# Optimization experiments

Measured on AMD Instinct MI355X. Metric: run time of the kernel, lower is better.

## Reference

```python
import jax, jax.numpy as jnp
import numpy as np

C_IN, C_OUT, K = 64, 64, 3
KK = K * K


def _conv3x3(x, w, b):
    # x: [B, Cin, H, W], w: [Cout, Cin, 3, 3], b: [Cout] or None. stride 1, pad 1.
    y = jax.lax.conv_general_dilated(
        x, w, window_strides=(1, 1), padding=((1, 1), (1, 1)),
        dimension_numbers=("NCHW", "OIHW", "NCHW"))
    if b is not None:
        y = y + b[None, :, None, None]
    return y


def _deform_conv2d(x, offset, mask, weight):
    # torchvision.ops.deform_conv2d with stride=1, pad=1, dilation=1, 1 offset group.
    # x: [B,C,H,W]; offset: [B,2*KK,H,W] (per-tap (dy,dx)); mask: [B,KK,H,W];
    # weight: [O,C,K,K]
    B, C, H, W = x.shape
    O = weight.shape[0]
    ky, kx = jnp.meshgrid(jnp.arange(K), jnp.arange(K), indexing="ij")
    hs = jnp.arange(H)
    ws = jnp.arange(W)
    # base sample positions per tap k=(ky*K+kx): [KK,H,W]
    base_y = (hs[:, None] - 1)[None] + ky.reshape(KK, 1, 1)
    base_x = (ws[None, :] - 1)[None] + kx.reshape(KK, 1, 1)
    off = offset.reshape(B, KK, 2, H, W)
    py = base_y[None].astype(x.dtype) + off[:, :, 0]  # [B,KK,H,W]
    px = base_x[None].astype(x.dtype) + off[:, :, 1]

    y0 = jnp.floor(py)
    x0 = jnp.floor(px)
    wy = py - y0  # bilinear fractional weights
    wx = px - x0
    y0i = y0.astype(jnp.int32)
    x0i = x0.astype(jnp.int32)

    imflat = x.reshape(B, C, H * W)

    def gather_b(im, idx):  # im: [C,HW], idx: [KK,H,W] -> [C,KK,H,W]
        return im[:, idx]

    val = jnp.zeros((B, C, KK, H, W), x.dtype)
    for dy, dx in ((0, 0), (0, 1), (1, 0), (1, 1)):
        yc = y0i + dy
        xc = x0i + dx
        valid = ((yc >= 0) & (yc < H) & (xc >= 0) & (xc < W)).astype(x.dtype)
        cw = (wy if dy else (1.0 - wy)) * (wx if dx else (1.0 - wx)) * valid
        idx = jnp.clip(yc, 0, H - 1) * W + jnp.clip(xc, 0, W - 1)
        g = jax.vmap(gather_b)(imflat, idx)  # [B,C,KK,H,W]
        val = val + cw[:, None] * g
    val = val * mask[:, None]  # modulation
    # contract 9-tap patches with conv weight
    return jnp.einsum("bckhw,ock->bohw", val, weight.reshape(O, C, KK))


def setup_inputs() -> dict:
    key = jax.random.key(0)
    ks = jax.random.split(key, 8)
    B, H, W = 4, 96, 96
    cin2 = 2 * C_IN + 2
    frame_i = jax.random.normal(ks[0], (B, C_IN, H, W), jnp.float32)
    frame_j = jax.random.normal(ks[1], (B, C_IN, H, W), jnp.float32)
    flow_ij = jax.random.normal(ks[2], (B, 2, H, W), jnp.float32)
    # small random weights so offsets are nonzero (zero-init would degenerate)
    w_off = jax.random.normal(ks[3], (2 * KK, cin2, K, K), jnp.float32) * 0.01
    b_off = jax.random.normal(ks[4], (2 * KK,), jnp.float32) * 0.1
    w_mod = jax.random.normal(ks[5], (KK, cin2, K, K), jnp.float32) * 0.01
    b_mod = jax.random.normal(ks[6], (KK,), jnp.float32) * 0.1
    w_reg = jax.random.normal(ks[7], (C_OUT, C_IN, K, K), jnp.float32) * (1.0 / np.sqrt(C_IN * KK))
    return {"frame_i": frame_i, "frame_j": frame_j, "flow_ij": flow_ij,
            "w_off": w_off, "b_off": b_off, "w_mod": w_mod, "b_mod": b_mod,
            "w_reg": w_reg}


def reference(frame_i, frame_j, flow_ij, w_off, b_off, w_mod, b_mod, w_reg):
    offset_input = jnp.concatenate([frame_i, frame_j, flow_ij], axis=1)
    offset = _conv3x3(offset_input, w_off, b_off)            # [B,2*KK,H,W]
    modulator = 2.0 * jax.nn.sigmoid(_conv3x3(offset_input, w_mod, b_mod))  # [B,KK,H,W]
    return _deform_conv2d(frame_j, offset, modulator, w_reg)
```

## Files before the change

### kernel.cpp

```cpp
#include <hip/hip_runtime.h>
#include <math.h>

#define BB   4
#define HH   96
#define WW   96
#define HW   (HH * WW)
#define CIN  64
#define COUT 64
#define C2B  192
#define NROW (BB * HW)
#define ZROW NROW
#define NSTRIP (NROW / 16)
#define BPX3 (NSTRIP / 8)
#define NA   (9 * 5 * 2 * 512)
#define NW   (9 * 2 * 4 * 512)
#define PXB2 (NROW / 32)
#define PWBLK 324
#define TSX  35
#define RS   20

typedef short v8s __attribute__((ext_vector_type(8)));
typedef float v4f __attribute__((ext_vector_type(4)));

__device__ __forceinline__ unsigned short f2bf(float f) {
    unsigned u = __float_as_uint(f);
    return (unsigned short)((u + 0x7FFFu + ((u >> 16) & 1u)) >> 16);
}
__device__ __forceinline__ unsigned pack2(float a, float b) {
    return (unsigned)f2bf(a) | ((unsigned)f2bf(b) << 16);
}
__device__ __forceinline__ unsigned bil2(unsigned a, unsigned b, unsigned c,
                                         unsigned d, float w00, float w01,
                                         float w10, float w11) {
    float lo = w00 * __uint_as_float(a << 16) + w01 * __uint_as_float(b << 16)
             + w10 * __uint_as_float(c << 16) + w11 * __uint_as_float(d << 16);
    float hi = w00 * __uint_as_float(a & 0xffff0000u)
             + w01 * __uint_as_float(b & 0xffff0000u)
             + w10 * __uint_as_float(c & 0xffff0000u)
             + w11 * __uint_as_float(d & 0xffff0000u);
    return pack2(lo, hi);
}

__global__ __launch_bounds__(256) void prep_kernel(
    const float* __restrict__ fi, const float* __restrict__ fj,
    const float* __restrict__ fl, const float* __restrict__ w_off,
    const float* __restrict__ w_mod, const float* __restrict__ w_reg,
    unsigned short* __restrict__ xt, unsigned short* __restrict__ wa2f,
    unsigned short* __restrict__ wb2f)
{
    int blk = blockIdx.x;
    if (blk < PXB2) {
        __shared__ __align__(16) unsigned tile[64 * TSX];
        int tid = threadIdx.x;
        int p = tid & 63, cg = tid >> 6;
        int u = blk >> 1, half = blk & 1;
        int r0 = u * 64;
        int b = r0 / HW;
        int hw = r0 - b * HW + p;
        uint4* dst = (uint4*)(xt + (size_t)r0 * C2B);
        if (half == 0) {
            const float* pi = fi + (size_t)b * CIN * HW + hw;
#pragma unroll
            for (int d = 0; d < 8; ++d) {
                int c = cg * 16 + 2 * d;
                tile[p * TSX + cg * 8 + d] =
                    pack2(pi[(size_t)c * HW], pi[(size_t)(c + 1) * HW]);
            }
            __syncthreads();
#pragma unroll
            for (int i = 0; i < 2; ++i) {
                int gq = i * 256 + tid;
                int rl = gq >> 3, c4 = gq & 7;
                const unsigned* s = &tile[rl * TSX + c4 * 4];
                uint4 v = {s[0], s[1], s[2], s[3]};
                dst[rl * 24 + c4] = v;
            }
        } else {
            const float* pj = fj + (size_t)b * CIN * HW + hw;
#pragma unroll
            for (int d = 0; d < 8; ++d) {
                int c = cg * 16 + 2 * d;
                tile[p * TSX + cg * 8 + d] =
                    pack2(pj[(size_t)c * HW], pj[(size_t)(c + 1) * HW]);
            }
            if (cg == 0) {
                const float* pf = fl + (size_t)b * 2 * HW + hw;
                tile[p * TSX + 32] = pack2(pf[0], pf[HW]);
            }
            __syncthreads();
#pragma unroll
            for (int i = 0; i < 4; ++i) {
                int gq = i * 256 + tid;
                int rl = gq >> 4, c4 = gq & 15;
                uint4 v = {0u, 0u, 0u, 0u};
                if (c4 < 8) {
                    const unsigned* s = &tile[rl * TSX + c4 * 4];
                    v.x = s[0]; v.y = s[1]; v.z = s[2]; v.w = s[3];
                } else if (c4 == 8) {
                    v.x = tile[rl * TSX + 32];
                }
                dst[rl * 24 + 8 + c4] = v;
            }
        }
    } else if (blk < PXB2 + PWBLK) {
        int e = (blk - PXB2) * 256 + threadIdx.x;
        if (e < NA) {
            int t  = e / 5120;
            int r1 = e - t * 5120;
            int ks = r1 >> 10;
            int r2 = r1 & 1023;
            int nt = r2 >> 9;
            int l9 = r2 & 511;
            int l  = l9 >> 3, ee = l9 & 7;
            int m  = l & 15, g = l >> 4;
            int oc = nt * 16 + m;
            int ch = ks * 32 + g * 8 + ee;
            float v = 0.0f;
            if (oc < 27 && ch < 130) {
                if (oc < 18) v = w_off[((size_t)oc * 130 + ch) * 9 + t];
                else         v = w_mod[((size_t)(oc - 18) * 130 + ch) * 9 + t];
            }
            wa2f[e] = f2bf(v);
        } else {
            int e2 = e - NA;
            if (e2 < NW) {
                int k  = e2 >> 12;
                int r1 = e2 & 4095;
                int ks = r1 >> 11;
                int r2 = r1 & 2047;
                int nt = r2 >> 9;
                int l9 = r2 & 511;
                int l  = l9 >> 3, ee = l9 & 7;
                int m  = l & 15, g = l >> 4;
                int o  = nt * 16 + m;
                int c  = ks * 32 + g * 8 + ee;
                wb2f[e2] = f2bf(w_reg[((size_t)o * 64 + c) * 9 + k]);
            }
        }
    } else {
        if (threadIdx.x < 24) {
            uint4 z = {0u, 0u, 0u, 0u};
            ((uint4*)(xt + (size_t)ZROW * C2B))[threadIdx.x] = z;
        }
    }
}

__global__ __launch_bounds__(256, 2) void fused_kernel(
    const unsigned short* __restrict__ xt,
    const unsigned short* __restrict__ wa2f,
    const unsigned short* __restrict__ wb2f,
    const float* __restrict__ b_off, const float* __restrict__ b_mod,
    float* __restrict__ out)
{
    __shared__ float lraw[16 * 28];
    __shared__ __align__(16) float red[4][64 * RS];

    int l = threadIdx.x & 63;
    int wid = __builtin_amdgcn_readfirstlane(threadIdx.x >> 6);
    int m = l & 15, g = l >> 4;
    int strip = (blockIdx.x & 7) * BPX3 + (blockIdx.x >> 3);
    int b = strip / (HW / 16);
    int hw0 = (strip - b * (HW / 16)) * 16;
    int hw = hw0 + m;
    int x = hw % WW, y = hw / WW;
    int t0 = wid * 2;
    int ntap = (wid == 3) ? 3 : 2;

    v8s afr[3][5];
#pragma unroll
    for (int ti = 0; ti < 3; ++ti) {
        if (ti < ntap) {
            int t = t0 + ti;
            int ty = t / 3, tx = t - 3 * ty;
            int yy = y + ty - 1, xx = x + tx - 1;
            bool ok = ((unsigned)yy < HH) && ((unsigned)xx < WW);
            int row = ok ? (b * HW + yy * WW + xx) : ZROW;
            const unsigned short* ar = xt + (size_t)row * C2B + g * 8;
#pragma unroll
            for (int ks = 0; ks < 5; ++ks)
                afr[ti][ks] = *(const v8s*)(ar + ks * 32);
        }
    }
    __builtin_amdgcn_sched_barrier(0);

    v4f acc0 = {0.f, 0.f, 0.f, 0.f};
    v4f acc1 = {0.f, 0.f, 0.f, 0.f};
#pragma unroll
    for (int ti = 0; ti < 3; ++ti) {
        if (ti < ntap) {
            int t = t0 + ti;
#pragma unroll
            for (int ks = 0; ks < 5; ++ks) {
                const unsigned short* wp =
                    wa2f + ((size_t)((t * 5 + ks) * 2)) * 512 + l * 8;
                v8s b0 = *(const v8s*)(wp);
                v8s b1 = *(const v8s*)(wp + 512);
                acc0 = __builtin_amdgcn_mfma_f32_16x16x32_bf16(afr[ti][ks], b0, acc0, 0, 0, 0);
                acc1 = __builtin_amdgcn_mfma_f32_16x16x32_bf16(afr[ti][ks], b1, acc1, 0, 0, 0);
            }
        }
    }

    if (wid != 0) {
        float* rb = &red[wid][l * RS];
        *(v4f*)(rb + 0) = acc0;
        *(v4f*)(rb + 4) = acc1;
    }
    __syncthreads();
    if (wid == 0) {
#pragma unroll
        for (int sw = 1; sw < 4; ++sw) {
            const float* rb = &red[sw][l * RS];
            acc0 += *(const v4f*)(rb + 0);
            acc1 += *(const v4f*)(rb + 4);
        }
        float v0[4] = {acc0.x, acc0.y, acc0.z, acc0.w};
        float v1[4] = {acc1.x, acc1.y, acc1.z, acc1.w};
        float bo0 = b_off[m];
        int oc1 = 16 + m;
#pragma unroll
        for (int r = 0; r < 4; ++r)
            lraw[(g * 4 + r) * 28 + m] = v0[r] + bo0;
        if (oc1 < 18) {
            float bo1 = b_off[oc1];
#pragma unroll
            for (int r = 0; r < 4; ++r)
                lraw[(g * 4 + r) * 28 + oc1] = v1[r] + bo1;
        } else if (oc1 < 27) {
            float bm = b_mod[oc1 - 18];
#pragma unroll
            for (int r = 0; r < 4; ++r)
                lraw[(g * 4 + r) * 28 + oc1] =
                    2.0f / (1.0f + expf(-(v1[r] + bm)));
        }
    }
    __syncthreads();

    float cw[3][4];
    uint4 gbuf[3][8];
#pragma unroll
    for (int ti = 0; ti < 3; ++ti) {
        if (ti < ntap) {
            int k = t0 + ti;
            int ky = k / 3, kx = k - 3 * ky;
            float dy = lraw[m * 28 + 2 * k];
            float dx = lraw[m * 28 + 2 * k + 1];
            float mm = lraw[m * 28 + 18 + k];

            float py = (float)(y - 1 + ky) + dy;
            float px = (float)(x - 1 + kx) + dx;
            float fy = floorf(py), fx = floorf(px);
            int   y0 = (int)fy,    x0 = (int)fx;
            float wy = py - fy,    wx = px - fx;
            int   y1 = y0 + 1,     x1 = x0 + 1;

            bool y0v = (y0 >= 0) && (y0 < HH);
            bool y1v = (y1 >= 0) && (y1 < HH);
            bool x0v = (x0 >= 0) && (x0 < WW);
            bool x1v = (x1 >= 0) && (x1 < WW);

            cw[ti][0] = (1.f - wy) * (1.f - wx) * ((y0v && x0v) ? mm : 0.f);
            cw[ti][1] = (1.f - wy) * wx         * ((y0v && x1v) ? mm : 0.f);
            cw[ti][2] = wy * (1.f - wx)         * ((y1v && x0v) ? mm : 0.f);
            cw[ti][3] = wy * wx                 * ((y1v && x1v) ? mm : 0.f);

            int y0c = min(max(y0, 0), HH - 1), y1c = min(max(y1, 0), HH - 1);
            int x0c = min(max(x0, 0), WW - 1), x1c = min(max(x1, 0), WW - 1);
            int rb = b * HW;
            const unsigned short* r00 = xt + (size_t)(rb + y0c * WW + x0c) * C2B + 64 + g * 8;
            const unsigned short* r01 = xt + (size_t)(rb + y0c * WW + x1c) * C2B + 64 + g * 8;
            const unsigned short* r10 = xt + (size_t)(rb + y1c * WW + x0c) * C2B + 64 + g * 8;
            const unsigned short* r11 = xt + (size_t)(rb + y1c * WW + x1c) * C2B + 64 + g * 8;
#pragma unroll
            for (int ks = 0; ks < 2; ++ks) {
                gbuf[ti][ks * 4 + 0] = *(const uint4*)(r00 + ks * 32);
                gbuf[ti][ks * 4 + 1] = *(const uint4*)(r01 + ks * 32);
                gbuf[ti][ks * 4 + 2] = *(const uint4*)(r10 + ks * 32);
                gbuf[ti][ks * 4 + 3] = *(const uint4*)(r11 + ks * 32);
            }
        }
    }
    __builtin_amdgcn_sched_barrier(0);

    v4f acc[4];
#pragma unroll
    for (int nt = 0; nt < 4; ++nt) acc[nt] = (v4f){0.f, 0.f, 0.f, 0.f};

#pragma unroll
    for (int ti = 0; ti < 3; ++ti) {
        if (ti < ntap) {
            int k = t0 + ti;
            float w00 = cw[ti][0], w01 = cw[ti][1];
            float w10 = cw[ti][2], w11 = cw[ti][3];
            v8s afrag[2];
#pragma unroll
            for (int ks = 0; ks < 2; ++ks) {
                uint4 u00 = gbuf[ti][ks * 4 + 0];
                uint4 u01 = gbuf[ti][ks * 4 + 1];
                uint4 u10 = gbuf[ti][ks * 4 + 2];
                uint4 u11 = gbuf[ti][ks * 4 + 3];
                uint4 ov;
                ov.x = bil2(u00.x, u01.x, u10.x, u11.x, w00, w01, w10, w11);
                ov.y = bil2(u00.y, u01.y, u10.y, u11.y, w00, w01, w10, w11);
                ov.z = bil2(u00.z, u01.z, u10.z, u11.z, w00, w01, w10, w11);
                ov.w = bil2(u00.w, u01.w, u10.w, u11.w, w00, w01, w10, w11);
                afrag[ks] = __builtin_bit_cast(v8s, ov);
            }
#pragma unroll
            for (int nt = 0; nt < 4; ++nt) {
#pragma unroll
                for (int ks = 0; ks < 2; ++ks) {
                    const unsigned short* wp =
                        wb2f + ((size_t)((k * 2 + ks) * 4 + nt)) * 512 + l * 8;
                    v8s bb = *(const v8s*)wp;
                    acc[nt] = __builtin_amdgcn_mfma_f32_16x16x32_bf16(
                        afrag[ks], bb, acc[nt], 0, 0, 0);
                }
            }
        }
    }

    {
        float* rb = &red[wid][l * RS];
        *(v4f*)(rb + 0)  = acc[0];
        *(v4f*)(rb + 4)  = acc[1];
        *(v4f*)(rb + 8)  = acc[2];
        *(v4f*)(rb + 12) = acc[3];
    }
    __syncthreads();
    {
        v4f s = {0.f, 0.f, 0.f, 0.f};
#pragma unroll
        for (int sw = 0; sw < 4; ++sw)
            s += *(const v4f*)(&red[sw][l * RS + wid * 4]);
        float* op = out + ((size_t)(b * COUT + wid * 16 + m)) * HW + hw0 + g * 4;
        *(v4f*)op = s;
    }
}

extern "C" void kernel_launch(void* const* d_in, const int* in_sizes, int n_in,
                              void* d_out, int out_size, void* d_ws, size_t ws_size,
                              hipStream_t stream)
{
    const float* frame_i = (const float*)d_in[0];
    const float* frame_j = (const float*)d_in[1];
    const float* flow_ij = (const float*)d_in[2];
    const float* w_off   = (const float*)d_in[3];
    const float* b_off   = (const float*)d_in[4];
    const float* w_mod   = (const float*)d_in[5];
    const float* b_mod   = (const float*)d_in[6];
    const float* w_reg   = (const float*)d_in[7];
    float* out = (float*)d_out;

    unsigned short* xt   = (unsigned short*)d_ws;
    unsigned short* wa2f = xt + (size_t)(NROW + 1) * C2B;
    unsigned short* wb2f = wa2f + NA;

    prep_kernel<<<PXB2 + PWBLK + 1, 256, 0, stream>>>(
        frame_i, frame_j, flow_ij, w_off, w_mod, w_reg, xt, wa2f, wb2f);

    fused_kernel<<<NSTRIP, 256, 0, stream>>>(
        xt, wa2f, wb2f, b_off, b_mod, out);
}
```

Baseline: 134.8 us.

## Stage offset-conv input halo patch in LDS and interleave frame_j channel layout

The offset/modulator conv now cooperatively loads a 3-row by 18-pixel halo patch of the packed input into shared memory once per block. Each wave then reads its tap fragments from LDS, replacing per-lane global loads that fetched overlapping neighbours up to nine times. The prep kernel also permutes the frame_j channel chunks so each lane's two bilinear gather chunks sit in 32 contiguous bytes, improving coalescing of the deformable gathers. The cost is about 17 KB more shared memory per block, which may affect occupancy, plus an extra block-wide barrier before the first MFMA loop.

```diff
diff --git a/kernel.cpp b/kernel.cpp
--- a/kernel.cpp
+++ b/kernel.cpp
@@ -18,6 +18,7 @@
 #define PWBLK 324
 #define TSX  35
 #define RS   20
+#define PR   55
 
 typedef short v8s __attribute__((ext_vector_type(8)));
 typedef float v4f __attribute__((ext_vector_type(4)));
@@ -99,7 +100,8 @@
                 } else if (c4 == 8) {
                     v.x = tile[rl * TSX + 32];
                 }
-                dst[rl * 24 + 8 + c4] = v;
+                int pc4 = (c4 < 8) ? ((c4 & 3) * 2 + (c4 >> 2)) : c4;
+                dst[rl * 24 + 8 + pc4] = v;
             }
         }
     } else if (blk < PXB2 + PWBLK) {
@@ -152,6 +154,7 @@
     const float* __restrict__ b_off, const float* __restrict__ b_mod,
     float* __restrict__ out)
 {
+    __shared__ __align__(16) uint4 patch4[20 * PR];
     __shared__ float lraw[16 * 28];
     __shared__ __align__(16) float red[4][64 * RS];
 
@@ -163,40 +166,47 @@
     int hw0 = (strip - b * (HW / 16)) * 16;
     int hw = hw0 + m;
     int x = hw % WW, y = hw / WW;
+    int y0b = hw0 / WW, x0b = hw0 - y0b * WW;
     int t0 = wid * 2;
     int ntap = (wid == 3) ? 3 : 2;
 
-    v8s afr[3][5];
+#pragma unroll
+    for (int i = 0; i < 5; ++i) {
+        int item = i * 256 + threadIdx.x;
+        if (item < 1080) {
+            int run = item / 360;
+            int rem = item - run * 360;
+            int r18 = rem / 20;
+            int c8  = rem - r18 * 20;
+            int yy = y0b + run - 1;
+            int xx = x0b - 1 + r18;
+            bool ok = ((unsigned)yy < HH) && ((unsigned)xx < WW);
+            uint4 v = {0u, 0u, 0u, 0u};
+            if (ok)
+                v = ((const uint4*)(xt + (size_t)(b * HW + yy * WW + xx) * C2B))[c8];
+            patch4[c8 * PR + run * 18 + r18] = v;
+        }
+    }
+    __syncthreads();
+
+    v4f acc0 = {0.f, 0.f, 0.f, 0.f};
+    v4f acc1 = {0.f, 0.f, 0.f, 0.f};
 #pragma unroll
     for (int ti = 0; ti < 3; ++ti) {
         if (ti < ntap) {
             int t = t0 + ti;
-            int ty = t / 3, tx = t - 3 * ty;
-            int yy = y + ty - 1, xx = x + tx - 1;
-            bool ok = ((unsigned)yy < HH) && ((unsigned)xx < WW);
-            int row = ok ? (b * HW + yy * WW + xx) : ZROW;
-            const unsigned short* ar = xt + (size_t)row * C2B + g * 8;
-#pragma unroll
-            for (int ks = 0; ks < 5; ++ks)
-                afr[ti][ks] = *(const v8s*)(ar + ks * 32);
-        }
-    }
-    __builtin_amdgcn_sched_barrier(0);
-
-    v4f acc0 = {0.f, 0.f, 0.f, 0.f};
-    v4f acc1 = {0.f, 0.f, 0.f, 0.f};
-#pragma unroll
-    for (int ti = 0; ti < 3; ++ti) {
-        if (ti < ntap) {
-            int t = t0 + ti;
+            int r = (t / 3) * 18 + (t % 3) + m;
 #pragma unroll
             for (int ks = 0; ks < 5; ++ks) {
+                int c8 = (ks == 0) ? g : (ks == 1) ? 4 + g
+                       : (ks == 2) ? 8 + 2 * g : (ks == 3) ? 9 + 2 * g : 16 + g;
+                v8s a = *(const v8s*)&patch4[c8 * PR + r];
                 const unsigned short* wp =
                     wa2f + ((size_t)((t * 5 + ks) * 2)) * 512 + l * 8;
                 v8s b0 = *(const v8s*)(wp);
                 v8s b1 = *(const v8s*)(wp + 512);
-                acc0 = __builtin_amdgcn_mfma_f32_16x16x32_bf16(afr[ti][ks], b0, acc0, 0, 0, 0);
-                acc1 = __builtin_amdgcn_mfma_f32_16x16x32_bf16(afr[ti][ks], b1, acc1, 0, 0, 0);
+                acc0 = __builtin_amdgcn_mfma_f32_16x16x32_bf16(a, b0, acc0, 0, 0, 0);
+                acc1 = __builtin_amdgcn_mfma_f32_16x16x32_bf16(a, b1, acc1, 0, 0, 0);
             }
         }
     }
@@ -267,16 +277,16 @@
             int y0c = min(max(y0, 0), HH - 1), y1c = min(max(y1, 0), HH - 1);
             int x0c = min(max(x0, 0), WW - 1), x1c = min(max(x1, 0), WW - 1);
             int rb = b * HW;
-            const unsigned short* r00 = xt + (size_t)(rb + y0c * WW + x0c) * C2B + 64 + g * 8;
-            const unsigned short* r01 = xt + (size_t)(rb + y0c * WW + x1c) * C2B + 64 + g * 8;
-            const unsigned short* r10 = xt + (size_t)(rb + y1c * WW + x0c) * C2B + 64 + g * 8;
-            const unsigned short* r11 = xt + (size_t)(rb + y1c * WW + x1c) * C2B + 64 + g * 8;
+            const unsigned short* r00 = xt + (size_t)(rb + y0c * WW + x0c) * C2B + 64 + g * 16;
+            const unsigned short* r01 = xt + (size_t)(rb + y0c * WW + x1c) * C2B + 64 + g * 16;
+            const unsigned short* r10 = xt + (size_t)(rb + y1c * WW + x0c) * C2B + 64 + g * 16;
+            const unsigned short* r11 = xt + (size_t)(rb + y1c * WW + x1c) * C2B + 64 + g * 16;
 #pragma unroll
             for (int ks = 0; ks < 2; ++ks) {
-                gbuf[ti][ks * 4 + 0] = *(const uint4*)(r00 + ks * 32);
-                gbuf[ti][ks * 4 + 1] = *(const uint4*)(r01 + ks * 32);
-                gbuf[ti][ks * 4 + 2] = *(const uint4*)(r10 + ks * 32);
-                gbuf[ti][ks * 4 + 3] = *(const uint4*)(r11 + ks * 32);
+                gbuf[ti][ks * 4 + 0] = *(const uint4*)(r00 + ks * 8);
+                gbuf[ti][ks * 4 + 1] = *(const uint4*)(r01 + ks * 8);
+                gbuf[ti][ks * 4 + 2] = *(const uint4*)(r10 + ks * 8);
+                gbuf[ti][ks * 4 + 3] = *(const uint4*)(r11 + ks * 8);
             }
         }
     }
```

Result: faster. 128.5 us (-4.6%).
